# Optimization experiments

Measured on AMD Instinct MI355X. Metric: run time of the kernel, lower is better.

The kernel has to match this reference:

```python
import jax, jax.numpy as jnp
import numpy as np

B, T, DIM, H, HD, K = 4, 2048, 1024, 16, 64, 4
QK = H * HD          # 1024
VD = 2 * H * HD      # 2048
EPS = 1e-5


def zrms(x, g):
    # zero-centered RMS norm with learned scale
    x = x - jnp.mean(x, axis=-1, keepdims=True)
    return x * jax.lax.rsqrt(jnp.mean(x * x, axis=-1, keepdims=True) + EPS) * g


def causal_dwconv(x, w):
    # x: [B,T,C], w: [K,1,C] (keras depthwise Conv1D kernel, groups=C)
    k = w.shape[0]
    return jax.lax.conv_general_dilated(
        x, w, window_strides=(1,), padding=[(k - 1, 0)],
        dimension_numbers=('NWC', 'WIO', 'NWC'),
        feature_group_count=x.shape[-1])


def setup_inputs() -> dict:
    key = jax.random.key(0)
    ks = jax.random.split(key, 12)
    s = lambda *sh: 1.0 / np.sqrt(sh[0])
    return {
        'x':  jax.random.normal(ks[0], (B, T, DIM), jnp.float32),
        'Wq': jax.random.normal(ks[1], (DIM, QK), jnp.float32) * s(DIM),
        'Wk': jax.random.normal(ks[2], (DIM, QK), jnp.float32) * s(DIM),
        'Wv': jax.random.normal(ks[3], (DIM, VD), jnp.float32) * s(DIM),
        'gq': jnp.ones((QK,), jnp.float32),
        'gk': jnp.ones((QK,), jnp.float32),
        'gv': jnp.ones((VD,), jnp.float32),
        'cq': jax.random.normal(ks[4], (K, 1, QK), jnp.float32) * 0.5,
        'ck': jax.random.normal(ks[5], (K, 1, QK), jnp.float32) * 0.5,
        'cv': jax.random.normal(ks[6], (K, 1, VD), jnp.float32) * 0.5,
        'Wa': jax.random.normal(ks[7], (DIM, H), jnp.float32) * s(DIM),
        'Wb': jax.random.normal(ks[8], (DIM, H), jnp.float32) * s(DIM),
        'Wo': jax.random.normal(ks[9], (VD, DIM), jnp.float32) * s(VD),
        'Wg': jax.random.normal(ks[10], (DIM, DIM), jnp.float32) * s(DIM),
    }


def reference(x, Wq, Wk, Wv, gq, gk, gv, cq, ck, cv, Wa, Wb, Wo, Wg):
    # 1) projections  2) zero-centered RMSNorm  3) causal depthwise conv (+silu)
    q = jax.nn.silu(causal_dwconv(zrms(x @ Wq, gq), cq))   # [B,T,QK]
    k = jax.nn.silu(causal_dwconv(zrms(x @ Wk, gk), ck))   # [B,T,QK]
    v = jax.nn.silu(causal_dwconv(zrms(x @ Wv, gv), cv))   # [B,T,VD]

    q = q.reshape(B, T, H, HD)
    k = k.reshape(B, T, H, HD)
    v = v.reshape(B, T, H, 2 * HD)

    # 4) per-head gating params
    alpha = jax.nn.sigmoid(x @ Wa)  # [B,T,H]
    beta = jax.nn.sigmoid(x @ Wb)   # [B,T,H]

    # 5) gated delta-rule recurrence over time (state S: [B,H,2*HD,HD])
    def step(S, inp):
        qt, kt, vt, at, bt = inp  # [B,H,HD],[B,H,HD],[B,H,2HD],[B,H],[B,H]
        a = at[..., None, None]
        upd = S + bt[..., None, None] * jnp.einsum('bhv,bhk->bhvk', vt, kt)
        S = a * upd + (1.0 - a) * S
        o = jnp.einsum('bhvk,bhk->bhv', S, qt)  # Q_t readout
        return S, o

    S0 = jnp.zeros((B, H, 2 * HD, HD), x.dtype)
    xs = (q.transpose(1, 0, 2, 3), k.transpose(1, 0, 2, 3),
          v.transpose(1, 0, 2, 3), alpha.transpose(1, 0, 2),
          beta.transpose(1, 0, 2))
    _, o = jax.lax.scan(step, S0, xs)          # o: [T,B,H,2HD]
    o = o.transpose(1, 0, 2, 3).reshape(B, T, VD)

    # 6) output projection + sigmoid output gate
    proj = o @ Wo                              # [B,T,DIM]
    return jax.nn.sigmoid(proj @ Wg) * proj
```

## Files before the change

kernel.cpp:

```cpp
#include <hip/hip_runtime.h>
#include <hip/hip_bf16.h>
#include <math.h>

#define RTOT 8192
#define TSEQ 2048

typedef __attribute__((ext_vector_type(8))) short short8;
typedef __attribute__((ext_vector_type(4))) float f32x4;
typedef unsigned short u16;
typedef unsigned int u32;

union U16x8 { uint4 v; u16 s[8]; };

__device__ __forceinline__ float sigmoidf_(float x) { return 1.f / (1.f + expf(-x)); }
__device__ __forceinline__ float bf2f(u16 v) { u32 u = ((u32)v) << 16; float f; __builtin_memcpy(&f, &u, 4); return f; }
__device__ __forceinline__ u16 f2bf(float f) {
  u32 u; __builtin_memcpy(&u, &f, 4);
  u32 r = (u + 0x7FFFu + ((u >> 16) & 1u)) >> 16;
  return (u16)r;
}
__device__ __forceinline__ void split2(float x, u16& h, u16& l) {
  u16 hh = f2bf(x);
  float hf = bf2f(hh);
  h = hh; l = f2bf(x - hf);
}

typedef const void __attribute__((address_space(1))) gvoid_t;
typedef void __attribute__((address_space(3))) lvoid_t;
__device__ __forceinline__ void gload_lds16(const void* g, void* l) {
  __builtin_amdgcn_global_load_lds((gvoid_t*)g, (lvoid_t*)l, 16, 0, 0);
}

__device__ __forceinline__ void xcd_remap(int& bx, int& by) {
  int gx = gridDim.x, nwg = gx * gridDim.y;
  int bid = blockIdx.y * gx + blockIdx.x;
  int cpx = nwg >> 3;
  int swz = (bid & 7) * cpx + (bid >> 3);
  bx = swz % gx; by = swz / gx;
}

template<int EPI>
__global__ __launch_bounds__(256) void gemm_sp(const u16* __restrict__ Ah, const u16* __restrict__ Al,
                                               const u16* __restrict__ Bh, const u16* __restrict__ Bl,
                                               float* __restrict__ Cf, u16* __restrict__ Ph,
                                               u16* __restrict__ Pl, const float* __restrict__ Pin,
                                               int M, int N, int K) {
  __shared__ u16 Ash[128 * 32], Asl[128 * 32];
  __shared__ u16 Bsh[128 * 32], Bsl[128 * 32];
  int bx, by; xcd_remap(bx, by);
  const int tid = threadIdx.x;
  const int l = tid & 63, w = tid >> 6;
  const int m0 = by * 128, n0 = bx * 128;
  const int wr = w >> 1, wc = w & 1;
  f32x4 acc[4][4] = {};
  const int srow = (w << 5) + (l >> 2);
  const int scol = (l & 3) << 3;
  const size_t gA = (size_t)(m0 + srow) * K + scol;
  const size_t gB = (size_t)(n0 + srow) * K + scol;
  const int lo0 = (w * 2 + 0) * 512, lo1 = (w * 2 + 1) * 512;
  const int arow = wr * 64 + (l & 15), brow = wc * 64 + (l & 15);
  const int koff = 8 * (l >> 4);
  for (int k0 = 0; k0 < K; k0 += 32) {
    gload_lds16(Ah + gA + k0, &Ash[lo0]);
    gload_lds16(Ah + gA + 16 * K + k0, &Ash[lo1]);
    gload_lds16(Al + gA + k0, &Asl[lo0]);
    gload_lds16(Al + gA + 16 * K + k0, &Asl[lo1]);
    gload_lds16(Bh + gB + k0, &Bsh[lo0]);
    gload_lds16(Bh + gB + 16 * K + k0, &Bsh[lo1]);
    gload_lds16(Bl + gB + k0, &Bsl[lo0]);
    gload_lds16(Bl + gB + 16 * K + k0, &Bsl[lo1]);
    __syncthreads();
    short8 afh[4], afl[4], bfh[4], bfl[4];
#pragma unroll
    for (int m = 0; m < 4; ++m) {
      afh[m] = *(const short8*)&Ash[(arow + m * 16) * 32 + koff];
      afl[m] = *(const short8*)&Asl[(arow + m * 16) * 32 + koff];
    }
#pragma unroll
    for (int n = 0; n < 4; ++n) {
      bfh[n] = *(const short8*)&Bsh[(brow + n * 16) * 32 + koff];
      bfl[n] = *(const short8*)&Bsl[(brow + n * 16) * 32 + koff];
    }
#pragma unroll
    for (int m = 0; m < 4; ++m)
#pragma unroll
      for (int n = 0; n < 4; ++n) {
        acc[m][n] = __builtin_amdgcn_mfma_f32_16x16x32_bf16(afh[m], bfh[n], acc[m][n], 0, 0, 0);
        acc[m][n] = __builtin_amdgcn_mfma_f32_16x16x32_bf16(afh[m], bfl[n], acc[m][n], 0, 0, 0);
        acc[m][n] = __builtin_amdgcn_mfma_f32_16x16x32_bf16(afl[m], bfh[n], acc[m][n], 0, 0, 0);
      }
    __syncthreads();
  }
  const int rbase = m0 + wr * 64 + 4 * (l >> 4);
  const int cbase = n0 + wc * 64 + (l & 15);
#pragma unroll
  for (int m = 0; m < 4; ++m)
#pragma unroll
    for (int n = 0; n < 4; ++n)
#pragma unroll
      for (int r = 0; r < 4; ++r) {
        size_t idx = (size_t)(rbase + m * 16 + r) * N + (cbase + n * 16);
        float v = acc[m][n][r];
        if (EPI == 0) {
          Cf[idx] = v;
        } else if (EPI == 1) {
          Cf[idx] = v;
          u16 h, lo; split2(v, h, lo);
          Ph[idx] = h; Pl[idx] = lo;
        } else {
          Cf[idx] = Pin[idx] * sigmoidf_(v);
        }
      }
}

__global__ __launch_bounds__(256) void transcast_sp(const float* __restrict__ W,
                                                    u16* __restrict__ Wth, u16* __restrict__ Wtl,
                                                    int K, int N) {
  __shared__ float t[32][33];
  const int n0 = blockIdx.x * 32, k0 = blockIdx.y * 32;
  const int c = threadIdx.x & 31, rq = threadIdx.x >> 5;
#pragma unroll
  for (int i = 0; i < 4; ++i) t[rq * 4 + i][c] = W[(size_t)(k0 + rq * 4 + i) * N + n0 + c];
  __syncthreads();
#pragma unroll
  for (int i = 0; i < 4; ++i) {
    float v = t[c][rq * 4 + i];
    u16 h, lo; split2(v, h, lo);
    size_t idx = (size_t)(n0 + rq * 4 + i) * K + k0 + c;
    Wth[idx] = h; Wtl[idx] = lo;
  }
}

__global__ __launch_bounds__(256) void castx_sp(const float* __restrict__ x,
                                                u16* __restrict__ xh, u16* __restrict__ xl) {
  size_t i = (size_t)blockIdx.x * 256 + threadIdx.x;
  float4 v = ((const float4*)x)[i];
  ushort4 hh, ll;
  split2(v.x, hh.x, ll.x); split2(v.y, hh.y, ll.y);
  split2(v.z, hh.z, ll.z); split2(v.w, hh.w, ll.w);
  ((ushort4*)xh)[i] = hh; ((ushort4*)xl)[i] = ll;
}

template<int C>
__global__ __launch_bounds__(256) void stats_kernel(const float* __restrict__ base,
                                                    float* __restrict__ st) {
  constexpr int NQ = C / 1024;
  __shared__ float red[4];
  const int tid = threadIdx.x;
  const size_t row = blockIdx.x;
  const float* x = base + row * 2048;
  float4 v[NQ];
  float s = 0.f;
#pragma unroll
  for (int i = 0; i < NQ; ++i) {
    v[i] = *(const float4*)(x + tid*4 + i*1024);
    s += v[i].x + v[i].y + v[i].z + v[i].w;
  }
#pragma unroll
  for (int o = 32; o > 0; o >>= 1) s += __shfl_xor(s, o, 64);
  if ((tid & 63) == 0) red[tid >> 6] = s;
  __syncthreads();
  const float mean = (red[0]+red[1]+red[2]+red[3]) * (1.f / C);
  __syncthreads();
  float ss = 0.f;
#pragma unroll
  for (int i = 0; i < NQ; ++i) {
    float a = v[i].x - mean, b = v[i].y - mean, c = v[i].z - mean, d = v[i].w - mean;
    ss += a*a + b*b + c*c + d*d;
  }
#pragma unroll
  for (int o = 32; o > 0; o >>= 1) ss += __shfl_xor(ss, o, 64);
  if ((tid & 63) == 0) red[tid >> 6] = ss;
  __syncthreads();
  if (tid == 0) {
    st[row * 2] = mean;
    st[row * 2 + 1] = rsqrtf((red[0]+red[1]+red[2]+red[3]) * (1.f / C) + 1e-5f);
  }
}

template<int C, int GSCALE>
__global__ __launch_bounds__(256) void conv_ns(const float* __restrict__ zn,
                                               const float* __restrict__ st,
                                               const float* __restrict__ w,
                                               const float* __restrict__ g,
                                               const float* __restrict__ gab,
                                               u16* __restrict__ oh,
                                               u16* __restrict__ ol) {
  const size_t idx = (size_t)blockIdx.x * 256 + threadIdx.x;
  const int c = (int)(idx % (C/4)) * 4;
  const int row = (int)(idx / (C/4));
  const int t = row % TSEQ;
  float4 g4 = *(const float4*)(g + c);
  float4 acc = {0.f, 0.f, 0.f, 0.f};
#pragma unroll
  for (int d = 0; d < 4; ++d) {
    if (t - d >= 0) {
      const int r2 = row - d;
      const float mean = st[r2 * 2], rstd = st[r2 * 2 + 1];
      float4 xv = *(const float4*)(zn + (size_t)r2 * 2048 + c);
      float4 wv = *(const float4*)(w + (size_t)(3 - d) * C + c);
      acc.x = fmaf((xv.x - mean) * rstd * g4.x, wv.x, acc.x);
      acc.y = fmaf((xv.y - mean) * rstd * g4.y, wv.y, acc.y);
      acc.z = fmaf((xv.z - mean) * rstd * g4.z, wv.z, acc.z);
      acc.w = fmaf((xv.w - mean) * rstd * g4.w, wv.w, acc.w);
    }
  }
  float a0 = acc.x * sigmoidf_(acc.x);
  float a1 = acc.y * sigmoidf_(acc.y);
  float a2 = acc.z * sigmoidf_(acc.z);
  float a3 = acc.w * sigmoidf_(acc.w);
  if (GSCALE) {
    float gv = gab[(size_t)row * 16 + (c >> 7)];
    a0 *= gv; a1 *= gv; a2 *= gv; a3 *= gv;
  }
  ushort4 hh, ll;
  split2(a0, hh.x, ll.x); split2(a1, hh.y, ll.y);
  split2(a2, hh.z, ll.z); split2(a3, hh.w, ll.w);
  *(ushort4*)(oh + (size_t)row * C + c) = hh;
  *(ushort4*)(ol + (size_t)row * C + c) = ll;
}

__global__ __launch_bounds__(256) void gab_kernel(const float* __restrict__ x,
                                                  const float* __restrict__ Wa,
                                                  const float* __restrict__ Wb,
                                                  float* __restrict__ gout) {
  __shared__ float xs[1024];
  __shared__ float partial[256];
  const int tid = threadIdx.x;
  const size_t row = blockIdx.x;
  *(float4*)(&xs[tid*4]) = *(const float4*)(x + row*1024 + tid*4);
  __syncthreads();
  const int h = tid & 31;
  const int seg = tid >> 5;
  const float* W = (h < 16) ? Wa : Wb;
  const int col = h & 15;
  float s = 0.f;
  const int k0 = seg * 128;
  for (int k = 0; k < 128; ++k) s = fmaf(xs[k0 + k], W[(size_t)(k0 + k) * 16 + col], s);
  partial[tid] = s;
  __syncthreads();
  if (tid < 32) {
    float t2 = 0.f;
#pragma unroll
    for (int j = 0; j < 8; ++j) t2 += partial[j*32 + tid];
    partial[tid] = t2;
  }
  __syncthreads();
  if (tid < 16)
    gout[row*16 + tid] = sigmoidf_(partial[tid]) * sigmoidf_(partial[tid + 16]);
}

__global__ __launch_bounds__(256) void scan_kernel(const u16* __restrict__ kh,
                                                   const u16* __restrict__ kl,
                                                   const u16* __restrict__ vgh,
                                                   const u16* __restrict__ vgl,
                                                   u16* __restrict__ Sph,
                                                   u16* __restrict__ Spl) {
  __shared__ float Ks[64][36];
  __shared__ float Vs[64][36];
  const int tid = threadIdx.x;
  const int bid = blockIdx.x;
  const int kq = bid & 1, vq = (bid >> 1) & 3, h = (bid >> 3) & 15, b = bid >> 7;
  const size_t rb = (size_t)b * TSEQ;
  const int vd_t = tid >> 3, kd0 = (tid & 7) * 4;
  float S[4] = {};
  const int sr = tid >> 2;
  const int cc0 = (tid & 3) * 8;
  for (int c = 0; c < 32; ++c) {
    {
      size_t koffg = (rb + (size_t)c * 64 + sr) * 1024 + h * 64 + kq * 32 + cc0;
      U16x8 a0, b0;
      a0.v = *(const uint4*)(kh + koffg);
      b0.v = *(const uint4*)(kl + koffg);
#pragma unroll
      for (int j = 0; j < 8; ++j) Ks[sr][cc0 + j] = bf2f(a0.s[j]) + bf2f(b0.s[j]);
      size_t voffg = (rb + (size_t)c * 64 + sr) * 2048 + h * 128 + vq * 32 + cc0;
      U16x8 va, vb;
      va.v = *(const uint4*)(vgh + voffg);
      vb.v = *(const uint4*)(vgl + voffg);
#pragma unroll
      for (int j = 0; j < 8; ++j) Vs[sr][cc0 + j] = bf2f(va.s[j]) + bf2f(vb.s[j]);
    }
    {
      size_t spc = (((size_t)(b * 16 + h) * 32) + c) * 8192
                 + (size_t)(vq * 32 + vd_t) * 64 + kq * 32 + kd0;
      ushort4 h0, l0;
      split2(S[0], h0.x, l0.x); split2(S[1], h0.y, l0.y);
      split2(S[2], h0.z, l0.z); split2(S[3], h0.w, l0.w);
      *(ushort4*)(Sph + spc) = h0;
      *(ushort4*)(Spl + spc) = l0;
    }
    __syncthreads();
    for (int s = 0; s < 64; ++s) {
      float vv = Vs[s][vd_t];
      float kv[4];
      *(float4*)kv = *(const float4*)&Ks[s][kd0];
#pragma unroll
      for (int j = 0; j < 4; ++j) S[j] = fmaf(vv, kv[j], S[j]);
    }
    __syncthreads();
  }
}

__global__ __launch_bounds__(256) void pass2_sp(const u16* __restrict__ qh,
                                                const u16* __restrict__ ql,
                                                const u16* __restrict__ kh,
                                                const u16* __restrict__ vgh,
                                                const u16* __restrict__ Sph,
                                                const u16* __restrict__ Spl,
                                                u16* __restrict__ oh,
                                                u16* __restrict__ ol) {
  __shared__ u16 Qsh[64 * 72];
  __shared__ u16 Qsl[64 * 72];
  __shared__ u16 Ksm[64 * 72];
  __shared__ u16 Am[64 * 72];
  __shared__ u16 Vth[128 * 72];
  const int tid = threadIdx.x;
  const int l = tid & 63, w = tid >> 6;
  const int bid = blockIdx.x;
  const int c = bid & 31, h = (bid >> 5) & 15, b = bid >> 9;
  const size_t rb = (size_t)b * TSEQ + c * 64;
  const int fr = l & 15, fq = l >> 4;
  {
    int r = tid >> 2, c0 = (tid & 3) * 16;
    size_t off = (rb + r) * 1024 + h * 64 + c0;
    *(uint4*)&Qsh[r * 72 + c0]     = *(const uint4*)(qh + off);
    *(uint4*)&Qsh[r * 72 + c0 + 8] = *(const uint4*)(qh + off + 8);
    *(uint4*)&Qsl[r * 72 + c0]     = *(const uint4*)(ql + off);
    *(uint4*)&Qsl[r * 72 + c0 + 8] = *(const uint4*)(ql + off + 8);
    *(uint4*)&Ksm[r * 72 + c0]     = *(const uint4*)(kh + off);
    *(uint4*)&Ksm[r * 72 + c0 + 8] = *(const uint4*)(kh + off + 8);
  }
  {
    int s = tid >> 2, vd0 = (tid & 3) * 32;
    size_t off = (rb + s) * 2048 + h * 128 + vd0;
#pragma unroll
    for (int m4 = 0; m4 < 4; ++m4) {
      U16x8 r_; r_.v = *(const uint4*)(vgh + off + m4 * 8);
#pragma unroll
      for (int j = 0; j < 8; ++j) Vth[(vd0 + m4 * 8 + j) * 72 + s] = r_.s[j];
    }
  }
  __syncthreads();
  short8 aqh[2], aql[2];
#pragma unroll
  for (int kk = 0; kk < 2; ++kk) {
    aqh[kk] = *(const short8*)&Qsh[(w * 16 + fr) * 72 + kk * 32 + 8 * fq];
    aql[kk] = *(const short8*)&Qsl[(w * 16 + fr) * 72 + kk * 32 + 8 * fq];
  }
  f32x4 accA[4] = {};
#pragma unroll
  for (int n = 0; n < 4; ++n)
#pragma unroll
    for (int kk = 0; kk < 2; ++kk) {
      short8 bk = *(const short8*)&Ksm[(n * 16 + fr) * 72 + kk * 32 + 8 * fq];
      accA[n] = __builtin_amdgcn_mfma_f32_16x16x32_bf16(aqh[kk], bk, accA[n], 0, 0, 0);
    }
#pragma unroll
  for (int n = 0; n < 4; ++n)
#pragma unroll
    for (int rr = 0; rr < 4; ++rr) {
      int tt = w * 16 + 4 * fq + rr;
      int s = n * 16 + fr;
      Am[tt * 72 + s] = f2bf((s <= tt) ? accA[n][rr] : 0.f);
    }
  __syncthreads();
  f32x4 acc[8] = {};
#pragma unroll
  for (int kk = 0; kk < 2; ++kk) {
    short8 aa = *(const short8*)&Am[(w * 16 + fr) * 72 + kk * 32 + 8 * fq];
#pragma unroll
    for (int n = 0; n < 8; ++n) {
      short8 bv = *(const short8*)&Vth[(n * 16 + fr) * 72 + kk * 32 + 8 * fq];
      acc[n] = __builtin_amdgcn_mfma_f32_16x16x32_bf16(aa, bv, acc[n], 0, 0, 0);
    }
  }
  const size_t spb = (((size_t)(b * 16 + h) * 32) + c) * 8192;
#pragma unroll
  for (int n = 0; n < 8; ++n)
#pragma unroll
    for (int kk = 0; kk < 2; ++kk) {
      size_t soff = spb + (size_t)(n * 16 + fr) * 64 + kk * 32 + 8 * fq;
      short8 bh_ = *(const short8*)(Sph + soff);
      short8 bl_ = *(const short8*)(Spl + soff);
      acc[n] = __builtin_amdgcn_mfma_f32_16x16x32_bf16(aqh[kk], bh_, acc[n], 0, 0, 0);
      acc[n] = __builtin_amdgcn_mfma_f32_16x16x32_bf16(aqh[kk], bl_, acc[n], 0, 0, 0);
      acc[n] = __builtin_amdgcn_mfma_f32_16x16x32_bf16(aql[kk], bh_, acc[n], 0, 0, 0);
    }
#pragma unroll
  for (int n = 0; n < 8; ++n)
#pragma unroll
    for (int rr = 0; rr < 4; ++rr) {
      int tt = w * 16 + 4 * fq + rr;
      int vd = n * 16 + fr;
      u16 hh, ll;
      split2(acc[n][rr], hh, ll);
      size_t off = (rb + tt) * 2048 + h * 128 + vd;
      oh[off] = hh; ol[off] = ll;
    }
}

extern "C" void kernel_launch(void* const* d_in, const int* in_sizes, int n_in,
                              void* d_out, int out_size, void* d_ws, size_t ws_size,
                              hipStream_t stream) {
  (void)in_sizes; (void)n_in; (void)out_size; (void)ws_size;
  const float* x  = (const float*)d_in[0];
  const float* Wq = (const float*)d_in[1];
  const float* Wk = (const float*)d_in[2];
  const float* Wv = (const float*)d_in[3];
  const float* gq = (const float*)d_in[4];
  const float* gk = (const float*)d_in[5];
  const float* gv = (const float*)d_in[6];
  const float* cq = (const float*)d_in[7];
  const float* ck = (const float*)d_in[8];
  const float* cv = (const float*)d_in[9];
  const float* Wa = (const float*)d_in[10];
  const float* Wb = (const float*)d_in[11];
  const float* Wo = (const float*)d_in[12];
  const float* Wg = (const float*)d_in[13];
  float* out = (float*)d_out;
  char* ws = (char*)d_ws;

  const size_t MiB = 1024 * 1024;
  u16* Wqk_h = (u16*)(ws + 0 * MiB);
  u16* Wqk_l = (u16*)(ws + 4 * MiB);
  u16* Wv_h  = (u16*)(ws + 8 * MiB);
  u16* Wv_l  = (u16*)(ws + 12 * MiB);
  u16* Wo_h  = (u16*)(ws + 16 * MiB);
  u16* Wo_l  = (u16*)(ws + 20 * MiB);
  u16* Wg_h  = (u16*)(ws + 24 * MiB);
  u16* Wg_l  = (u16*)(ws + 26 * MiB);
  float* gbuf = (float*)(ws + 28 * MiB);
  float* st_q = (float*)(ws + 28 * MiB + 524288);
  float* st_k = (float*)(ws + 28 * MiB + 524288 + 65536);
  float* st_v = (float*)(ws + 28 * MiB + 524288 + 131072);
  u16* x_h   = (u16*)(ws + 32 * MiB);
  u16* x_l   = (u16*)(ws + 48 * MiB);
  float* qk  = (float*)(ws + 64 * MiB);
  float* vbuf = (float*)(ws + 128 * MiB);
  u16* q_h = (u16*)(ws + 192 * MiB);
  u16* q_l = (u16*)(ws + 208 * MiB);
  u16* k_h = (u16*)(ws + 224 * MiB);
  u16* k_l = (u16*)(ws + 240 * MiB);
  u16* vg_h = (u16*)(ws + 64 * MiB);
  u16* vg_l = (u16*)(ws + 96 * MiB);
  u16* Sp_h = (u16*)(ws + 128 * MiB);
  u16* Sp_l = (u16*)(ws + 160 * MiB);
  u16* o_h  = (u16*)(ws + 32 * MiB);
  u16* o_l  = (u16*)d_out;
  float* proj = (float*)(ws + 64 * MiB);
  u16* p_h  = (u16*)(ws + 96 * MiB);
  u16* p_l  = (u16*)(ws + 112 * MiB);

  dim3 blk(256);
  castx_sp<<<dim3(8192), blk, 0, stream>>>(x, x_h, x_l);
  transcast_sp<<<dim3(32, 32), blk, 0, stream>>>(Wq, Wqk_h, Wqk_l, 1024, 1024);
  transcast_sp<<<dim3(32, 32), blk, 0, stream>>>(Wk, Wqk_h + 1024 * 1024, Wqk_l + 1024 * 1024, 1024, 1024);
  transcast_sp<<<dim3(64, 32), blk, 0, stream>>>(Wv, Wv_h, Wv_l, 1024, 2048);
  transcast_sp<<<dim3(32, 64), blk, 0, stream>>>(Wo, Wo_h, Wo_l, 2048, 1024);
  transcast_sp<<<dim3(32, 32), blk, 0, stream>>>(Wg, Wg_h, Wg_l, 1024, 1024);
  gab_kernel<<<dim3(8192), blk, 0, stream>>>(x, Wa, Wb, gbuf);
  gemm_sp<0><<<dim3(16, 64), blk, 0, stream>>>(x_h, x_l, Wqk_h, Wqk_l, qk, nullptr, nullptr, nullptr, 8192, 2048, 1024);
  gemm_sp<0><<<dim3(16, 64), blk, 0, stream>>>(x_h, x_l, Wv_h, Wv_l, vbuf, nullptr, nullptr, nullptr, 8192, 2048, 1024);
  stats_kernel<1024><<<dim3(8192), blk, 0, stream>>>(qk, st_q);
  stats_kernel<1024><<<dim3(8192), blk, 0, stream>>>(qk + 1024, st_k);
  stats_kernel<2048><<<dim3(8192), blk, 0, stream>>>(vbuf, st_v);
  conv_ns<1024, 0><<<dim3(8192), blk, 0, stream>>>(qk, st_q, cq, gq, nullptr, q_h, q_l);
  conv_ns<1024, 0><<<dim3(8192), blk, 0, stream>>>(qk + 1024, st_k, ck, gk, nullptr, k_h, k_l);
  conv_ns<2048, 1><<<dim3(16384), blk, 0, stream>>>(vbuf, st_v, cv, gv, gbuf, vg_h, vg_l);
  scan_kernel<<<dim3(512), blk, 0, stream>>>(k_h, k_l, vg_h, vg_l, Sp_h, Sp_l);
  pass2_sp<<<dim3(2048), blk, 0, stream>>>(q_h, q_l, k_h, vg_h, Sp_h, Sp_l, o_h, o_l);
  gemm_sp<1><<<dim3(8, 64), blk, 0, stream>>>(o_h, o_l, Wo_h, Wo_l, proj, p_h, p_l, nullptr, 8192, 1024, 2048);
  gemm_sp<2><<<dim3(8, 64), blk, 0, stream>>>(p_h, p_l, Wg_h, Wg_l, out, nullptr, nullptr, proj, 8192, 1024, 1024);
}
```

Before: 745.4 us.

## Merge QKV projections into one GEMM and fuse norm stats into conv

The separate QK and V projection GEMMs become one GEMM over a concatenated QKV weight, writing a single 4096-wide buffer. The three row-stats kernels are removed: each conv block handles one row and recomputes mean and rstd for the four causal taps with warp shuffles and shared-memory reductions, then applies the conv. This cuts kernel launches and avoids writing and re-reading the stats buffers. The cost is recomputing statistics four times per row, and the workspace layout is reshuffled, with vg_l now aliased onto the output buffer.

Result: faster. 718.0 us (-3.7%).

```diff
diff --git a/kernel.cpp b/kernel.cpp
--- a/kernel.cpp
+++ b/kernel.cpp
@@ -141,68 +141,80 @@
   ((ushort4*)xh)[i] = hh; ((ushort4*)xl)[i] = ll;
 }
 
-template<int C>
-__global__ __launch_bounds__(256) void stats_kernel(const float* __restrict__ base,
-                                                    float* __restrict__ st) {
-  constexpr int NQ = C / 1024;
-  __shared__ float red[4];
+template<int C, int GSCALE>
+__global__ __launch_bounds__(C / 4) void conv_fs(const float* __restrict__ zn,
+                                                 const float* __restrict__ w,
+                                                 const float* __restrict__ g,
+                                                 const float* __restrict__ gab,
+                                                 u16* __restrict__ oh,
+                                                 u16* __restrict__ ol) {
+  constexpr int NW = C / 256;
+  __shared__ float redA[NW * 4];
+  __shared__ float redB[NW * 4];
   const int tid = threadIdx.x;
-  const size_t row = blockIdx.x;
-  const float* x = base + row * 2048;
-  float4 v[NQ];
-  float s = 0.f;
-#pragma unroll
-  for (int i = 0; i < NQ; ++i) {
-    v[i] = *(const float4*)(x + tid*4 + i*1024);
-    s += v[i].x + v[i].y + v[i].z + v[i].w;
-  }
-#pragma unroll
-  for (int o = 32; o > 0; o >>= 1) s += __shfl_xor(s, o, 64);
-  if ((tid & 63) == 0) red[tid >> 6] = s;
-  __syncthreads();
-  const float mean = (red[0]+red[1]+red[2]+red[3]) * (1.f / C);
-  __syncthreads();
-  float ss = 0.f;
-#pragma unroll
-  for (int i = 0; i < NQ; ++i) {
-    float a = v[i].x - mean, b = v[i].y - mean, c = v[i].z - mean, d = v[i].w - mean;
-    ss += a*a + b*b + c*c + d*d;
-  }
-#pragma unroll
-  for (int o = 32; o > 0; o >>= 1) ss += __shfl_xor(ss, o, 64);
-  if ((tid & 63) == 0) red[tid >> 6] = ss;
-  __syncthreads();
-  if (tid == 0) {
-    st[row * 2] = mean;
-    st[row * 2 + 1] = rsqrtf((red[0]+red[1]+red[2]+red[3]) * (1.f / C) + 1e-5f);
-  }
-}
-
-template<int C, int GSCALE>
-__global__ __launch_bounds__(256) void conv_ns(const float* __restrict__ zn,
-                                               const float* __restrict__ st,
-                                               const float* __restrict__ w,
-                                               const float* __restrict__ g,
-                                               const float* __restrict__ gab,
-                                               u16* __restrict__ oh,
-                                               u16* __restrict__ ol) {
-  const size_t idx = (size_t)blockIdx.x * 256 + threadIdx.x;
-  const int c = (int)(idx % (C/4)) * 4;
-  const int row = (int)(idx / (C/4));
-  const int t = row % TSEQ;
+  const int row = blockIdx.x;
+  const int t = row & (TSEQ - 1);
+  const int c = tid * 4;
+  const int lane = tid & 63, wid = tid >> 6;
+  float4 xv[4];
+  float psum[4];
+#pragma unroll
+  for (int d = 0; d < 4; ++d) {
+    if (t - d >= 0) xv[d] = *(const float4*)(zn + (size_t)(row - d) * 4096 + c);
+    else { xv[d].x = 0.f; xv[d].y = 0.f; xv[d].z = 0.f; xv[d].w = 0.f; }
+    psum[d] = xv[d].x + xv[d].y + xv[d].z + xv[d].w;
+  }
+#pragma unroll
+  for (int d = 0; d < 4; ++d)
+#pragma unroll
+    for (int o = 32; o > 0; o >>= 1) psum[d] += __shfl_xor(psum[d], o, 64);
+  if (lane == 0) {
+    redA[wid * 4 + 0] = psum[0]; redA[wid * 4 + 1] = psum[1];
+    redA[wid * 4 + 2] = psum[2]; redA[wid * 4 + 3] = psum[3];
+  }
+  __syncthreads();
+  float mean[4];
+#pragma unroll
+  for (int d = 0; d < 4; ++d) {
+    float s = 0.f;
+#pragma unroll
+    for (int j = 0; j < NW; ++j) s += redA[j * 4 + d];
+    mean[d] = s * (1.f / C);
+  }
+  float psq[4];
+#pragma unroll
+  for (int d = 0; d < 4; ++d) {
+    float a = xv[d].x - mean[d], b = xv[d].y - mean[d];
+    float e = xv[d].z - mean[d], f = xv[d].w - mean[d];
+    psq[d] = a * a + b * b + e * e + f * f;
+  }
+#pragma unroll
+  for (int d = 0; d < 4; ++d)
+#pragma unroll
+    for (int o = 32; o > 0; o >>= 1) psq[d] += __shfl_xor(psq[d], o, 64);
+  if (lane == 0) {
+    redB[wid * 4 + 0] = psq[0]; redB[wid * 4 + 1] = psq[1];
+    redB[wid * 4 + 2] = psq[2]; redB[wid * 4 + 3] = psq[3];
+  }
+  __syncthreads();
+  float rstd[4];
+#pragma unroll
+  for (int d = 0; d < 4; ++d) {
+    float s = 0.f;
+#pragma unroll
+    for (int j = 0; j < NW; ++j) s += redB[j * 4 + d];
+    rstd[d] = rsqrtf(s * (1.f / C) + 1e-5f);
+  }
   float4 g4 = *(const float4*)(g + c);
-  float4 acc = {0.f, 0.f, 0.f, 0.f};
+  float4 acc; acc.x = 0.f; acc.y = 0.f; acc.z = 0.f; acc.w = 0.f;
 #pragma unroll
   for (int d = 0; d < 4; ++d) {
     if (t - d >= 0) {
-      const int r2 = row - d;
-      const float mean = st[r2 * 2], rstd = st[r2 * 2 + 1];
-      float4 xv = *(const float4*)(zn + (size_t)r2 * 2048 + c);
       float4 wv = *(const float4*)(w + (size_t)(3 - d) * C + c);
-      acc.x = fmaf((xv.x - mean) * rstd * g4.x, wv.x, acc.x);
-      acc.y = fmaf((xv.y - mean) * rstd * g4.y, wv.y, acc.y);
-      acc.z = fmaf((xv.z - mean) * rstd * g4.z, wv.z, acc.z);
-      acc.w = fmaf((xv.w - mean) * rstd * g4.w, wv.w, acc.w);
+      acc.x = fmaf((xv[d].x - mean[d]) * rstd[d] * g4.x, wv.x, acc.x);
+      acc.y = fmaf((xv[d].y - mean[d]) * rstd[d] * g4.y, wv.y, acc.y);
+      acc.z = fmaf((xv[d].z - mean[d]) * rstd[d] * g4.z, wv.z, acc.z);
+      acc.w = fmaf((xv[d].w - mean[d]) * rstd[d] * g4.w, wv.w, acc.w);
     }
   }
   float a0 = acc.x * sigmoidf_(acc.x);
@@ -422,52 +434,42 @@
   char* ws = (char*)d_ws;
 
   const size_t MiB = 1024 * 1024;
-  u16* Wqk_h = (u16*)(ws + 0 * MiB);
-  u16* Wqk_l = (u16*)(ws + 4 * MiB);
-  u16* Wv_h  = (u16*)(ws + 8 * MiB);
-  u16* Wv_l  = (u16*)(ws + 12 * MiB);
-  u16* Wo_h  = (u16*)(ws + 16 * MiB);
-  u16* Wo_l  = (u16*)(ws + 20 * MiB);
-  u16* Wg_h  = (u16*)(ws + 24 * MiB);
-  u16* Wg_l  = (u16*)(ws + 26 * MiB);
+  u16* Wqkv_h = (u16*)(ws + 0 * MiB);
+  u16* Wqkv_l = (u16*)(ws + 8 * MiB);
+  u16* Wo_h   = (u16*)(ws + 16 * MiB);
+  u16* Wo_l   = (u16*)(ws + 20 * MiB);
+  u16* Wg_h   = (u16*)(ws + 24 * MiB);
+  u16* Wg_l   = (u16*)(ws + 26 * MiB);
   float* gbuf = (float*)(ws + 28 * MiB);
-  float* st_q = (float*)(ws + 28 * MiB + 524288);
-  float* st_k = (float*)(ws + 28 * MiB + 524288 + 65536);
-  float* st_v = (float*)(ws + 28 * MiB + 524288 + 131072);
-  u16* x_h   = (u16*)(ws + 32 * MiB);
-  u16* x_l   = (u16*)(ws + 48 * MiB);
-  float* qk  = (float*)(ws + 64 * MiB);
-  float* vbuf = (float*)(ws + 128 * MiB);
+  u16* x_h    = (u16*)(ws + 32 * MiB);
+  u16* x_l    = (u16*)(ws + 48 * MiB);
+  float* qkv  = (float*)(ws + 64 * MiB);
   u16* q_h = (u16*)(ws + 192 * MiB);
   u16* q_l = (u16*)(ws + 208 * MiB);
   u16* k_h = (u16*)(ws + 224 * MiB);
   u16* k_l = (u16*)(ws + 240 * MiB);
-  u16* vg_h = (u16*)(ws + 64 * MiB);
-  u16* vg_l = (u16*)(ws + 96 * MiB);
-  u16* Sp_h = (u16*)(ws + 128 * MiB);
-  u16* Sp_l = (u16*)(ws + 160 * MiB);
-  u16* o_h  = (u16*)(ws + 32 * MiB);
+  u16* vg_h = (u16*)(ws + 32 * MiB);
+  u16* vg_l = (u16*)d_out;
+  u16* Sp_h = (u16*)(ws + 96 * MiB);
+  u16* Sp_l = (u16*)(ws + 128 * MiB);
+  u16* o_h  = (u16*)(ws + 64 * MiB);
   u16* o_l  = (u16*)d_out;
-  float* proj = (float*)(ws + 64 * MiB);
-  u16* p_h  = (u16*)(ws + 96 * MiB);
-  u16* p_l  = (u16*)(ws + 112 * MiB);
+  float* proj = (float*)(ws + 96 * MiB);
+  u16* p_h  = (u16*)(ws + 128 * MiB);
+  u16* p_l  = (u16*)(ws + 144 * MiB);
 
   dim3 blk(256);
   castx_sp<<<dim3(8192), blk, 0, stream>>>(x, x_h, x_l);
-  transcast_sp<<<dim3(32, 32), blk, 0, stream>>>(Wq, Wqk_h, Wqk_l, 1024, 1024);
-  transcast_sp<<<dim3(32, 32), blk, 0, stream>>>(Wk, Wqk_h + 1024 * 1024, Wqk_l + 1024 * 1024, 1024, 1024);
-  transcast_sp<<<dim3(64, 32), blk, 0, stream>>>(Wv, Wv_h, Wv_l, 1024, 2048);
+  transcast_sp<<<dim3(32, 32), blk, 0, stream>>>(Wq, Wqkv_h, Wqkv_l, 1024, 1024);
+  transcast_sp<<<dim3(32, 32), blk, 0, stream>>>(Wk, Wqkv_h + 1024 * 1024, Wqkv_l + 1024 * 1024, 1024, 1024);
+  transcast_sp<<<dim3(64, 32), blk, 0, stream>>>(Wv, Wqkv_h + 2048 * 1024, Wqkv_l + 2048 * 1024, 1024, 2048);
   transcast_sp<<<dim3(32, 64), blk, 0, stream>>>(Wo, Wo_h, Wo_l, 2048, 1024);
   transcast_sp<<<dim3(32, 32), blk, 0, stream>>>(Wg, Wg_h, Wg_l, 1024, 1024);
   gab_kernel<<<dim3(8192), blk, 0, stream>>>(x, Wa, Wb, gbuf);
-  gemm_sp<0><<<dim3(16, 64), blk, 0, stream>>>(x_h, x_l, Wqk_h, Wqk_l, qk, nullptr, nullptr, nullptr, 8192, 2048, 1024);
-  gemm_sp<0><<<dim3(16, 64), blk, 0, stream>>>(x_h, x_l, Wv_h, Wv_l, vbuf, nullptr, nullptr, nullptr, 8192, 2048, 1024);
-  stats_kernel<1024><<<dim3(8192), blk, 0, stream>>>(qk, st_q);
-  stats_kernel<1024><<<dim3(8192), blk, 0, stream>>>(qk + 1024, st_k);
-  stats_kernel<2048><<<dim3(8192), blk, 0, stream>>>(vbuf, st_v);
-  conv_ns<1024, 0><<<dim3(8192), blk, 0, stream>>>(qk, st_q, cq, gq, nullptr, q_h, q_l);
-  conv_ns<1024, 0><<<dim3(8192), blk, 0, stream>>>(qk + 1024, st_k, ck, gk, nullptr, k_h, k_l);
-  conv_ns<2048, 1><<<dim3(16384), blk, 0, stream>>>(vbuf, st_v, cv, gv, gbuf, vg_h, vg_l);
+  gemm_sp<0><<<dim3(32, 64), blk, 0, stream>>>(x_h, x_l, Wqkv_h, Wqkv_l, qkv, nullptr, nullptr, nullptr, 8192, 4096, 1024);
+  conv_fs<1024, 0><<<dim3(8192), dim3(256), 0, stream>>>(qkv, cq, gq, nullptr, q_h, q_l);
+  conv_fs<1024, 0><<<dim3(8192), dim3(256), 0, stream>>>(qkv + 1024, ck, gk, nullptr, k_h, k_l);
+  conv_fs<2048, 1><<<dim3(8192), dim3(512), 0, stream>>>(qkv + 2048, cv, gv, gbuf, vg_h, vg_l);
   scan_kernel<<<dim3(512), blk, 0, stream>>>(k_h, k_l, vg_h, vg_l, Sp_h, Sp_l);
   pass2_sp<<<dim3(2048), blk, 0, stream>>>(q_h, q_l, k_h, vg_h, Sp_h, Sp_l, o_h, o_l);
   gemm_sp<1><<<dim3(8, 64), blk, 0, stream>>>(o_h, o_l, Wo_h, Wo_l, proj, p_h, p_l, nullptr, 8192, 1024, 2048);
```
